# Kernel optimization log

Measured on AMD Instinct MI355X. Metric: run time of the kernel, lower is better.

The kernel has to match this reference:

```python
import jax, jax.numpy as jnp
import numpy as np

T, B, D, H = 1024, 64, 256, 256


def setup_inputs() -> dict:
    key = jax.random.key(0)
    ks = jax.random.split(key, 7)
    u = lambda k, shape: jax.random.uniform(k, shape, jnp.float32, -0.1, 0.1)
    x = jax.random.normal(ks[0], (T, B, D), dtype=jnp.float32)
    # gate order along last axis: f, g, i, o (each block of width H)
    fwd_W = u(ks[1], (D, 4 * H))
    fwd_U = u(ks[2], (H, 4 * H))
    fwd_b = u(ks[3], (4 * H,))
    bwd_W = u(ks[4], (D, 4 * H))
    bwd_U = u(ks[5], (H, 4 * H))
    bwd_b = u(ks[6], (4 * H,))
    return {"x": x, "fwd_W": fwd_W, "fwd_U": fwd_U, "fwd_b": fwd_b,
            "bwd_W": bwd_W, "bwd_U": bwd_U, "bwd_b": bwd_b}


def _lstm_scan(x, W, U, b):
    # x: [T, B, D]; returns (hs [T,B,H], h_last [B,H])
    Bsz = x.shape[1]
    h0 = jnp.zeros((Bsz, H), x.dtype)
    c0 = jnp.zeros((Bsz, H), x.dtype)
    xW = x @ W  # precompute input projections: [T, B, 4H]

    def step(carry, xw_t):
        h, c = carry
        z = xw_t + h @ U + b  # [B, 4H]
        f = jax.nn.sigmoid(z[:, 0 * H:1 * H])
        g = jnp.tanh(z[:, 1 * H:2 * H])
        i = jax.nn.sigmoid(z[:, 2 * H:3 * H])
        o = jax.nn.sigmoid(z[:, 3 * H:4 * H])
        c_new = c * f + g * i
        h_new = o * jnp.tanh(c_new)
        return (h_new, c_new), h_new

    (h_last, _), hs = jax.lax.scan(step, (h0, c0), xW)
    return hs, h_last


def reference(x, fwd_W, fwd_U, fwd_b, bwd_W, bwd_U, bwd_b):
    hs_f, h_f = _lstm_scan(x, fwd_W, fwd_U, fwd_b)
    hs_b_rev, h_b = _lstm_scan(x[::-1], bwd_W, bwd_U, bwd_b)
    hs_b = hs_b_rev[::-1]
    output = jnp.concatenate([hs_f, hs_b], axis=-1)  # [T, B, 2H]
    return (output, h_f, h_b)
```

## Files before the change

### kernel.cpp

```cpp
#include <hip/hip_runtime.h>

#define T_STEPS 1024
#define BATCH   64
#define NDIM    256
#define HID     256
#define G4      1024

typedef short bf16x8 __attribute__((ext_vector_type(8)));
typedef float f32x4  __attribute__((ext_vector_type(4)));
typedef unsigned short u16;

#define XW_ELEMS ((size_t)2 * T_STEPS * BATCH * G4)
#define UT_ELEMS ((size_t)2 * 4 * 65536)

__device__ __forceinline__ float b2f(u16 v) {
  union { unsigned u; float f; } c; c.u = ((unsigned)v) << 16; return c.f;
}
__device__ __forceinline__ u16 f2b(float f) {
  union { float f; unsigned u; } c; c.f = f;
  unsigned u = c.u;
  u += 0x7fffu + ((u >> 16) & 1u);
  return (u16)(u >> 16);
}
__device__ __forceinline__ float sigm(float x) {
  float e = __expf(-x);
  return __builtin_amdgcn_rcpf(1.0f + e);
}
__device__ __forceinline__ float tanh_f(float x) {
  return 2.0f * sigm(2.0f * x) - 1.0f;
}

__global__ __launch_bounds__(1024) void build_ut(
    const float* __restrict__ U0, const float* __restrict__ U1,
    u16* __restrict__ UT)
{
  const int d = blockIdx.x >> 2;
  const int g = blockIdx.x & 3;
  const float* __restrict__ U = d ? U1 : U0;
  const int w = threadIdx.x >> 6, lane = threadIdx.x & 63;
  const int q = lane >> 4, c15 = lane & 15;
  u16* dst = UT + ((size_t)d * 4 + g) * 65536;
  #pragma unroll
  for (int kf = 0; kf < 8; ++kf) {
    bf16x8 v;
    #pragma unroll
    for (int j = 0; j < 8; ++j)
      v[j] = (short)f2b(U[(size_t)(kf * 32 + q * 8 + j) * G4 + g * 256 + w * 16 + c15]);
    ((bf16x8*)dst)[((w * 8 + kf) << 6) + lane] = v;
  }
}

__global__ __launch_bounds__(256, 2) void xw_gemm(
    const float* __restrict__ x,
    const float* __restrict__ W0, const float* __restrict__ W1,
    const float* __restrict__ b0, const float* __restrict__ b1,
    u16* __restrict__ xw)
{
  const int d  = blockIdx.y >> 4;
  const int n0 = (blockIdx.y & 15) * 64;
  const int t0 = blockIdx.x * 32;
  const float* __restrict__ W    = d ? W1 : W0;
  const float* __restrict__ bias = d ? b1 : b0;
  const int lane = threadIdx.x & 63;
  const int wv   = threadIdx.x >> 6;
  const int q    = lane >> 4;
  const int c15  = lane & 15;

  bf16x8 uf[4][8];
  #pragma unroll
  for (int ct = 0; ct < 4; ++ct) {
    const int col = n0 + ct * 16 + c15;
    #pragma unroll
    for (int kf = 0; kf < 8; ++kf) {
      #pragma unroll
      for (int j = 0; j < 8; ++j)
        uf[ct][kf][j] = (short)f2b(W[(size_t)(kf * 32 + q * 8 + j) * G4 + col]);
    }
  }
  float bc[4];
  #pragma unroll
  for (int ct = 0; ct < 4; ++ct) bc[ct] = bias[n0 + ct * 16 + c15];

  __shared__ __align__(16) u16 Alds[64 * 256];

  for (int t = t0; t < t0 + 32; ++t) {
    __syncthreads();
    const float* xt = x + (size_t)t * BATCH * NDIM;
    #pragma unroll
    for (int i = 0; i < 8; ++i) {
      int g = (int)threadIdx.x + 256 * i;
      int r = g >> 5, c = g & 31;
      const float* src = xt + r * 256 + c * 8;
      bf16x8 v;
      #pragma unroll
      for (int j = 0; j < 8; ++j) v[j] = (short)f2b(src[j]);
      int cs = (c & 16) | ((c ^ (r & 15)) & 15);
      ((bf16x8*)Alds)[r * 32 + cs] = v;
    }
    __syncthreads();

    bf16x8 af[8];
    const int arow = wv * 16 + c15;
    #pragma unroll
    for (int kf = 0; kf < 8; ++kf) {
      int c = kf * 4 + q;
      int cs = (c & 16) | ((c ^ c15) & 15);
      af[kf] = ((const bf16x8*)Alds)[arow * 32 + cs];
    }

    f32x4 acc[4];
    #pragma unroll
    for (int ct = 0; ct < 4; ++ct) acc[ct] = (f32x4){0.f, 0.f, 0.f, 0.f};
    #pragma unroll
    for (int kf = 0; kf < 8; ++kf) {
      #pragma unroll
      for (int ct = 0; ct < 4; ++ct)
        acc[ct] = __builtin_amdgcn_mfma_f32_16x16x32_bf16(af[kf], uf[ct][kf], acc[ct], 0, 0, 0);
    }

    u16* dst = xw + (((size_t)d * T_STEPS + t) * 4 + wv) * 16384;
    #pragma unroll
    for (int ct = 0; ct < 4; ++ct) {
      int ncol = n0 + ct * 16;
      int g2 = ncol >> 8, w2 = (ncol >> 4) & 15;
      union { u16 s[4]; uint2 v; } pk;
      #pragma unroll
      for (int r = 0; r < 4; ++r) pk.s[r] = f2b(acc[ct][r] + bc[ct]);
      *(uint2*)(dst + (size_t)(w2 * 64 + q * 16 + c15) * 16 + g2 * 4) = pk.v;
    }
  }
}

__global__ __launch_bounds__(1024) void lstm_scan_fast(
    const u16* __restrict__ xw, const u16* __restrict__ UT,
    float* __restrict__ out)
{
  extern __shared__ __align__(16) u16 dynlds[];
  const int d  = blockIdx.x >> 2;
  const int bt = blockIdx.x & 3;
  const int tid  = threadIdx.x;
  const int w    = tid >> 6;
  const int lane = tid & 63;
  const int q    = lane >> 4;
  const int c15  = lane & 15;

  const u16* __restrict__ UTd = UT + (size_t)d * 4 * 65536;

  bf16x8 uf0[8], uf1[8];
  const bf16x8* UTf = (const bf16x8*)UTd;
  #pragma unroll
  for (int kf = 0; kf < 8; ++kf) {
    uf0[kf] = UTf[       ((w * 8 + kf) << 6) + lane];
    uf1[kf] = UTf[8192 + ((w * 8 + kf) << 6) + lane];
  }

  {
    const int4* src = (const int4*)(UTd + 2 * 65536);
    int4* dstl = (int4*)(dynlds + 8192);
    for (int i = tid; i < 8192; i += 1024) dstl[i] = src[i];
    for (int i = tid; i < 8192; i += 1024) dynlds[i] = 0;
  }

  const int4* __restrict__ Uo4 = (const int4*)(UTd + 3 * 65536);
  const int obase = (w << 9) | lane;
  const char* uib_base = (const char*)(dynlds + 8192) + (size_t)obase * 16;

  int afo[8];
  #pragma unroll
  for (int kf = 0; kf < 8; ++kf) {
    int cc = kf * 4 + q;
    int cs = (cc & 16) | ((cc ^ c15) & 15);
    afo[kf] = (c15 * 32 + cs) * 16;
  }
  const int colv = w * 16 + c15;
  int hwo[4];
  #pragma unroll
  for (int r = 0; r < 4; ++r) {
    int row = q * 4 + r;
    int cch = colv >> 3;
    int cs = (cch & 16) | ((cch ^ row) & 15);
    hwo[r] = ((row * 32 + cs) * 8 + (colv & 7)) * 2;
  }

  float cst[4] = {0.f, 0.f, 0.f, 0.f};
  __syncthreads();

  const int rowbase = bt * 16;
  const size_t hlast_base = (size_t)T_STEPS * BATCH * (2 * HID) + (size_t)d * BATCH * HID;
  const int t_first = d ? (T_STEPS - 1) : 0;

  const long xw_stride = d ? -(long)(4 * 16384) : (long)(4 * 16384);
  const u16* xwp = xw + (((size_t)d * T_STEPS + t_first) * 4 + bt) * 16384 + (size_t)tid * 16;
  union I4x2 { int4 v[2]; u16 s[16]; };
  I4x2 xn;
  xn.v[0] = ((const int4*)xwp)[0];
  xn.v[1] = ((const int4*)xwp)[1];
  xwp += xw_stride;

  int4 ofr[3];
  ofr[0] = Uo4[obase];
  ofr[1] = Uo4[obase + 64];

  float* outp = out + (size_t)(t_first * BATCH + rowbase + q * 4) * (2 * HID)
              + (size_t)d * HID + colv;
  const long out_stride = d ? -(long)(BATCH * 2 * HID) : (long)(BATCH * 2 * HID);

  int curoff = 0;
  for (int it = 0; it < T_STEPS; ++it) {
    f32x4 acc0 = { b2f(xn.s[0]),  b2f(xn.s[1]),  b2f(xn.s[2]),  b2f(xn.s[3])  };
    f32x4 acc1 = { b2f(xn.s[4]),  b2f(xn.s[5]),  b2f(xn.s[6]),  b2f(xn.s[7])  };
    f32x4 acc2 = { b2f(xn.s[8]),  b2f(xn.s[9]),  b2f(xn.s[10]), b2f(xn.s[11]) };
    f32x4 acc3 = { b2f(xn.s[12]), b2f(xn.s[13]), b2f(xn.s[14]), b2f(xn.s[15]) };

    if (it + 1 < T_STEPS) {
      xn.v[0] = ((const int4*)xwp)[0];
      xn.v[1] = ((const int4*)xwp)[1];
      xwp += xw_stride;
    }

    const char* hcb = (const char*)dynlds + curoff;
    bf16x8 afb[2], uib[2];
    afb[0] = *(const bf16x8*)(hcb + afo[0]);
    uib[0] = *(const bf16x8*)(uib_base);
    #pragma unroll
    for (int kf = 0; kf < 8; ++kf) {
      if (kf < 7) {
        afb[(kf + 1) & 1] = *(const bf16x8*)(hcb + afo[kf + 1]);
        uib[(kf + 1) & 1] = *(const bf16x8*)(uib_base + (kf + 1) * 1024);
      }
      if (kf < 6) ofr[(kf + 2) % 3] = Uo4[obase + ((kf + 2) << 6)];
      bf16x8 af = afb[kf & 1];
      union { int4 v; bf16x8 b; } oc; oc.v = ofr[kf % 3];
      acc0 = __builtin_amdgcn_mfma_f32_16x16x32_bf16(af, uf0[kf],     acc0, 0, 0, 0);
      acc1 = __builtin_amdgcn_mfma_f32_16x16x32_bf16(af, uf1[kf],     acc1, 0, 0, 0);
      acc2 = __builtin_amdgcn_mfma_f32_16x16x32_bf16(af, uib[kf & 1], acc2, 0, 0, 0);
      acc3 = __builtin_amdgcn_mfma_f32_16x16x32_bf16(af, oc.b,        acc3, 0, 0, 0);
    }
    ofr[0] = Uo4[obase];
    ofr[1] = Uo4[obase + 64];

    u16 hb[4]; float hv[4];
    #pragma unroll
    for (int r = 0; r < 4; ++r) {
      float fg = sigm(acc0[r]);
      float gg = tanh_f(acc1[r]);
      float ig = sigm(acc2[r]);
      float og = sigm(acc3[r]);
      float cn = cst[r] * fg + gg * ig;
      cst[r] = cn;
      hv[r] = og * tanh_f(cn);
      hb[r] = f2b(hv[r]);
    }

    const int nxtoff = curoff ^ 8192;
    char* hwp = (char*)dynlds + nxtoff;
    #pragma unroll
    for (int r = 0; r < 4; ++r) {
      *(u16*)(hwp + hwo[r]) = hb[r];
      outp[r * (2 * HID)] = hv[r];
    }
    outp += out_stride;
    if (it == T_STEPS - 1) {
      #pragma unroll
      for (int r = 0; r < 4; ++r)
        out[hlast_base + (size_t)(rowbase + q * 4 + r) * HID + colv] = hv[r];
    }
    curoff = nxtoff;
    __syncthreads();
  }
}

__global__ __launch_bounds__(1024) void lstm_scan_safe(
    const u16* __restrict__ xw,
    const float* __restrict__ U0, const float* __restrict__ U1,
    float* __restrict__ out)
{
  const int d  = blockIdx.x >> 2;
  const int bt = blockIdx.x & 3;
  const int tid  = threadIdx.x;
  const int w    = tid >> 6;
  const int lane = tid & 63;
  const int q    = lane >> 4;
  const int c15  = lane & 15;
  const float* __restrict__ U = d ? U1 : U0;

  bf16x8 uf[4][8];
  #pragma unroll
  for (int g = 0; g < 4; ++g) {
    const int col2 = g * 256 + w * 16 + c15;
    #pragma unroll
    for (int kf = 0; kf < 8; ++kf) {
      #pragma unroll
      for (int j = 0; j < 8; ++j)
        uf[g][kf][j] = (short)f2b(U[(size_t)(kf * 32 + q * 8 + j) * G4 + col2]);
    }
  }

  __shared__ __align__(16) u16 hbuf[2][16 * 256];
  for (int i = tid; i < 16 * 256; i += 1024) { hbuf[0][i] = 0; hbuf[1][i] = 0; }
  float cst[4] = {0.f, 0.f, 0.f, 0.f};
  __syncthreads();

  const int rowbase = bt * 16;
  const int col = w * 16 + c15;
  const size_t hlast_base = (size_t)T_STEPS * BATCH * (2 * HID) + (size_t)d * BATCH * HID;

  for (int it = 0; it < T_STEPS; ++it) {
    const int t = d ? (T_STEPS - 1 - it) : it;
    union { int4 v[2]; u16 s[16]; } xv;
    {
      const int4* xwt = (const int4*)(xw + ((((size_t)d * T_STEPS + t) * 4 + bt) * 1024 + tid) * 16);
      xv.v[0] = xwt[0]; xv.v[1] = xwt[1];
    }
    const int cur = it & 1;
    bf16x8 af[8];
    #pragma unroll
    for (int kf = 0; kf < 8; ++kf) {
      int cc = kf * 4 + q;
      int cs = (cc & 16) | ((cc ^ c15) & 15);
      af[kf] = ((const bf16x8*)hbuf[cur])[c15 * 32 + cs];
    }
    f32x4 acc[4];
    #pragma unroll
    for (int g = 0; g < 4; ++g) acc[g] = (f32x4){0.f, 0.f, 0.f, 0.f};
    #pragma unroll
    for (int kf = 0; kf < 8; ++kf)
      #pragma unroll
      for (int g = 0; g < 4; ++g)
        acc[g] = __builtin_amdgcn_mfma_f32_16x16x32_bf16(af[kf], uf[g][kf], acc[g], 0, 0, 0);

    u16 hb[4]; float hv[4];
    #pragma unroll
    for (int r = 0; r < 4; ++r) {
      float zf = acc[0][r] + b2f(xv.s[0 * 4 + r]);
      float zg = acc[1][r] + b2f(xv.s[1 * 4 + r]);
      float zi = acc[2][r] + b2f(xv.s[2 * 4 + r]);
      float zo = acc[3][r] + b2f(xv.s[3 * 4 + r]);
      float fg = sigm(zf), gg = tanh_f(zg), ig = sigm(zi), og = sigm(zo);
      float cn = cst[r] * fg + gg * ig;
      cst[r] = cn;
      hv[r] = og * tanh_f(cn);
      hb[r] = f2b(hv[r]);
    }
    const int nxt = cur ^ 1;
    #pragma unroll
    for (int r = 0; r < 4; ++r) {
      const int row = q * 4 + r;
      int cch = col >> 3;
      int cs = (cch & 16) | ((cch ^ row) & 15);
      hbuf[nxt][(row * 32 + cs) * 8 + (col & 7)] = hb[r];
      out[((size_t)t * BATCH + rowbase + row) * (2 * HID) + (size_t)d * HID + col] = hv[r];
    }
    if (it == T_STEPS - 1) {
      #pragma unroll
      for (int r = 0; r < 4; ++r)
        out[hlast_base + (size_t)(rowbase + q * 4 + r) * HID + col] = hv[r];
    }
    __syncthreads();
  }
}

extern "C" void kernel_launch(void* const* d_in, const int* in_sizes, int n_in,
                              void* d_out, int out_size, void* d_ws, size_t ws_size,
                              hipStream_t stream) {
  const float* x  = (const float*)d_in[0];
  const float* fW = (const float*)d_in[1];
  const float* fU = (const float*)d_in[2];
  const float* fb = (const float*)d_in[3];
  const float* bW = (const float*)d_in[4];
  const float* bU = (const float*)d_in[5];
  const float* bb = (const float*)d_in[6];
  u16*   xwbuf = (u16*)d_ws;
  u16*   UT    = (u16*)d_ws + XW_ELEMS;
  float* out   = (float*)d_out;

  const bool fast = ws_size >= (XW_ELEMS + UT_ELEMS) * sizeof(u16);

  dim3 g1(32, 32);
  xw_gemm<<<g1, 256, 0, stream>>>(x, fW, bW, fb, bb, xwbuf);
  if (fast) {
    build_ut<<<8, 1024, 0, stream>>>(fU, bU, UT);
    hipFuncSetAttribute((const void*)lstm_scan_fast,
                        hipFuncAttributeMaxDynamicSharedMemorySize, 147456);
    lstm_scan_fast<<<8, 1024, 147456, stream>>>(xwbuf, UT, out);
  } else {
    lstm_scan_safe<<<8, 1024, 0, stream>>>(xwbuf, fU, bU, out);
  }
}
```

Baseline: 3.915 ms.

## Fold log2e scaling into weights and fuse LSTM gate math with fewer reciprocals

Pre-scales W, U and bias by log2(e), or 2·log2(e) for the tanh gate, so the recurrent loop can call exp2 directly without a multiply. The gate nonlinearities and cell update are combined algebraically, cutting five reciprocals per element to two. The h values are packed to bf16 with a hardware pack instruction, and the U_o/U_i fragment prefetch is restructured to a deeper rotation that is issued before the loop barrier. The changes shorten the serial per-step critical path of the recurrence, at the cost of overflow clamping concerns and a change in rounding behaviour.

```diff
diff --git a/kernel.cpp b/kernel.cpp
--- a/kernel.cpp
+++ b/kernel.cpp
@@ -6,6 +6,9 @@
 #define HID     256
 #define G4      1024
 
+#define L2E  1.4426950408889634f
+#define L2E2 2.8853900817779268f
+
 typedef short bf16x8 __attribute__((ext_vector_type(8)));
 typedef float f32x4  __attribute__((ext_vector_type(4)));
 typedef unsigned short u16;
@@ -21,13 +24,6 @@
   unsigned u = c.u;
   u += 0x7fffu + ((u >> 16) & 1u);
   return (u16)(u >> 16);
-}
-__device__ __forceinline__ float sigm(float x) {
-  float e = __expf(-x);
-  return __builtin_amdgcn_rcpf(1.0f + e);
-}
-__device__ __forceinline__ float tanh_f(float x) {
-  return 2.0f * sigm(2.0f * x) - 1.0f;
 }
 
 __global__ __launch_bounds__(1024) void build_ut(
@@ -36,6 +32,7 @@
 {
   const int d = blockIdx.x >> 2;
   const int g = blockIdx.x & 3;
+  const float sc = (g == 1) ? L2E2 : L2E;
   const float* __restrict__ U = d ? U1 : U0;
   const int w = threadIdx.x >> 6, lane = threadIdx.x & 63;
   const int q = lane >> 4, c15 = lane & 15;
@@ -45,7 +42,7 @@
     bf16x8 v;
     #pragma unroll
     for (int j = 0; j < 8; ++j)
-      v[j] = (short)f2b(U[(size_t)(kf * 32 + q * 8 + j) * G4 + g * 256 + w * 16 + c15]);
+      v[j] = (short)f2b(sc * U[(size_t)(kf * 32 + q * 8 + j) * G4 + g * 256 + w * 16 + c15]);
     ((bf16x8*)dst)[((w * 8 + kf) << 6) + lane] = v;
   }
 }
@@ -67,19 +64,19 @@
   const int c15  = lane & 15;
 
   bf16x8 uf[4][8];
+  float bc[4];
   #pragma unroll
   for (int ct = 0; ct < 4; ++ct) {
     const int col = n0 + ct * 16 + c15;
+    const float sc = (((n0 + ct * 16) >> 8) == 1) ? L2E2 : L2E;
     #pragma unroll
     for (int kf = 0; kf < 8; ++kf) {
       #pragma unroll
       for (int j = 0; j < 8; ++j)
-        uf[ct][kf][j] = (short)f2b(W[(size_t)(kf * 32 + q * 8 + j) * G4 + col]);
-    }
-  }
-  float bc[4];
-  #pragma unroll
-  for (int ct = 0; ct < 4; ++ct) bc[ct] = bias[n0 + ct * 16 + c15];
+        uf[ct][kf][j] = (short)f2b(sc * W[(size_t)(kf * 32 + q * 8 + j) * G4 + col]);
+    }
+    bc[ct] = sc * bias[col];
+  }
 
   __shared__ __align__(16) u16 Alds[64 * 256];
 
@@ -200,6 +197,10 @@
   int4 ofr[3];
   ofr[0] = Uo4[obase];
   ofr[1] = Uo4[obase + 64];
+  ofr[2] = Uo4[obase + 128];
+
+  bf16x8 uib[2];
+  uib[0] = *(const bf16x8*)(uib_base);
 
   float* outp = out + (size_t)(t_first * BATCH + rowbase + q * 4) * (2 * HID)
               + (size_t)d * HID + colv;
@@ -219,18 +220,17 @@
     }
 
     const char* hcb = (const char*)dynlds + curoff;
-    bf16x8 afb[2], uib[2];
+    bf16x8 afb[2];
     afb[0] = *(const bf16x8*)(hcb + afo[0]);
-    uib[0] = *(const bf16x8*)(uib_base);
     #pragma unroll
     for (int kf = 0; kf < 8; ++kf) {
       if (kf < 7) {
         afb[(kf + 1) & 1] = *(const bf16x8*)(hcb + afo[kf + 1]);
         uib[(kf + 1) & 1] = *(const bf16x8*)(uib_base + (kf + 1) * 1024);
       }
-      if (kf < 6) ofr[(kf + 2) % 3] = Uo4[obase + ((kf + 2) << 6)];
+      union { int4 v; bf16x8 b; } oc; oc.v = ofr[kf % 3];
+      if (kf < 5) ofr[kf % 3] = Uo4[obase + ((kf + 3) << 6)];
       bf16x8 af = afb[kf & 1];
-      union { int4 v; bf16x8 b; } oc; oc.v = ofr[kf % 3];
       acc0 = __builtin_amdgcn_mfma_f32_16x16x32_bf16(af, uf0[kf],     acc0, 0, 0, 0);
       acc1 = __builtin_amdgcn_mfma_f32_16x16x32_bf16(af, uf1[kf],     acc1, 0, 0, 0);
       acc2 = __builtin_amdgcn_mfma_f32_16x16x32_bf16(af, uib[kf & 1], acc2, 0, 0, 0);
@@ -238,19 +238,28 @@
     }
     ofr[0] = Uo4[obase];
     ofr[1] = Uo4[obase + 64];
-
-    u16 hb[4]; float hv[4];
+    ofr[2] = Uo4[obase + 128];
+
+    float hv[4];
     #pragma unroll
     for (int r = 0; r < 4; ++r) {
-      float fg = sigm(acc0[r]);
-      float gg = tanh_f(acc1[r]);
-      float ig = sigm(acc2[r]);
-      float og = sigm(acc3[r]);
-      float cn = cst[r] * fg + gg * ig;
+      float ef = __builtin_amdgcn_exp2f(-acc0[r]);
+      float eg = __builtin_amdgcn_exp2f(-acc1[r]);
+      float ei = __builtin_amdgcn_exp2f(-acc2[r]);
+      float eo = __builtin_amdgcn_exp2f(-acc3[r]);
+      float A = 1.0f + ef, B = 1.0f + eg, C = 1.0f + ei, D = 1.0f - eg;
+      float BC  = B * C;
+      float num = cst[r] * BC + D * A;
+      float cn  = num * __builtin_amdgcn_rcpf(A * BC);
       cst[r] = cn;
-      hv[r] = og * tanh_f(cn);
-      hb[r] = f2b(hv[r]);
-    }
+      float ec = __builtin_amdgcn_exp2f(fminf(-L2E2 * cn, 30.0f));
+      float E = 1.0f + eo, F = 1.0f + ec, G = 1.0f - ec;
+      hv[r] = G * __builtin_amdgcn_rcpf(E * F);
+    }
+    unsigned p01, p23;
+    asm("v_cvt_pk_bf16_f32 %0, %1, %2" : "=v"(p01) : "v"(hv[0]), "v"(hv[1]));
+    asm("v_cvt_pk_bf16_f32 %0, %1, %2" : "=v"(p23) : "v"(hv[2]), "v"(hv[3]));
+    u16 hb[4] = { (u16)p01, (u16)(p01 >> 16), (u16)p23, (u16)(p23 >> 16) };
 
     const int nxtoff = curoff ^ 8192;
     char* hwp = (char*)dynlds + nxtoff;
@@ -266,6 +275,7 @@
         out[hlast_base + (size_t)(rowbase + q * 4 + r) * HID + colv] = hv[r];
     }
     curoff = nxtoff;
+    uib[0] = *(const bf16x8*)(uib_base);
     __syncthreads();
   }
 }
@@ -288,11 +298,12 @@
   #pragma unroll
   for (int g = 0; g < 4; ++g) {
     const int col2 = g * 256 + w * 16 + c15;
+    const float sc = (g == 1) ? L2E2 : L2E;
     #pragma unroll
     for (int kf = 0; kf < 8; ++kf) {
       #pragma unroll
       for (int j = 0; j < 8; ++j)
-        uf[g][kf][j] = (short)f2b(U[(size_t)(kf * 32 + q * 8 + j) * G4 + col2]);
+        uf[g][kf][j] = (short)f2b(sc * U[(size_t)(kf * 32 + q * 8 + j) * G4 + col2]);
     }
   }
 
@@ -336,10 +347,18 @@
       float zg = acc[1][r] + b2f(xv.s[1 * 4 + r]);
       float zi = acc[2][r] + b2f(xv.s[2 * 4 + r]);
       float zo = acc[3][r] + b2f(xv.s[3 * 4 + r]);
-      float fg = sigm(zf), gg = tanh_f(zg), ig = sigm(zi), og = sigm(zo);
-      float cn = cst[r] * fg + gg * ig;
+      float ef = __builtin_amdgcn_exp2f(-zf);
+      float eg = __builtin_amdgcn_exp2f(-zg);
+      float ei = __builtin_amdgcn_exp2f(-zi);
+      float eo = __builtin_amdgcn_exp2f(-zo);
+      float A = 1.0f + ef, B = 1.0f + eg, C = 1.0f + ei, D = 1.0f - eg;
+      float BC  = B * C;
+      float num = cst[r] * BC + D * A;
+      float cn  = num * __builtin_amdgcn_rcpf(A * BC);
       cst[r] = cn;
-      hv[r] = og * tanh_f(cn);
+      float ec = __builtin_amdgcn_exp2f(fminf(-L2E2 * cn, 30.0f));
+      float E = 1.0f + eo, F = 1.0f + ec, G = 1.0f - ec;
+      hv[r] = G * __builtin_amdgcn_rcpf(E * F);
       hb[r] = f2b(hv[r]);
     }
     const int nxt = cur ^ 1;
```

Result: slower. 4.420 ms (+12.9%).

## Pre-pack input weights to bf16 and restructure input projection GEMM around time tiles

Applied to the files above, without the earlier changes.

Adds a pre-pass that converts both input weight matrices to bf16 in the MFMA fragment layout, reusing the recurrent-weight packing kernel. A new projection kernel has each block load two timesteps of x into swizzled LDS once, keep the A fragments in registers, and loop over all 32 output column tiles for both directions. Weight fragments are read straight from global memory. The aim is to avoid repeatedly converting fp32 weights and re-reading x across blocks, at the cost of an extra launch, extra workspace and heavier register use.

```diff
diff --git a/kernel.cpp b/kernel.cpp
--- a/kernel.cpp
+++ b/kernel.cpp
@@ -12,6 +12,7 @@
 
 #define XW_ELEMS ((size_t)2 * T_STEPS * BATCH * G4)
 #define UT_ELEMS ((size_t)2 * 4 * 65536)
+#define WT_ELEMS UT_ELEMS
 
 __device__ __forceinline__ float b2f(u16 v) {
   union { unsigned u; float f; } c; c.u = ((unsigned)v) << 16; return c.f;
@@ -47,6 +48,93 @@
     for (int j = 0; j < 8; ++j)
       v[j] = (short)f2b(U[(size_t)(kf * 32 + q * 8 + j) * G4 + g * 256 + w * 16 + c15]);
     ((bf16x8*)dst)[((w * 8 + kf) << 6) + lane] = v;
+  }
+}
+
+__global__ __launch_bounds__(256, 2) void xw_gemm_v2(
+    const float* __restrict__ x,
+    const u16* __restrict__ WT,
+    const float* __restrict__ b0, const float* __restrict__ b1,
+    u16* __restrict__ xw)
+{
+  const int t0   = blockIdx.x * 2;
+  const int lane = threadIdx.x & 63;
+  const int wv   = threadIdx.x >> 6;
+  const int q    = lane >> 4;
+  const int c15  = lane & 15;
+
+  __shared__ __align__(16) u16 Alds[2 * 64 * 256];
+
+  #pragma unroll
+  for (int t01 = 0; t01 < 2; ++t01) {
+    const float* xt = x + (size_t)(t0 + t01) * BATCH * NDIM;
+    #pragma unroll
+    for (int i = 0; i < 8; ++i) {
+      int g = (int)threadIdx.x + 256 * i;
+      int r = g >> 5, c = g & 31;
+      const float* src = xt + r * 256 + c * 8;
+      bf16x8 v;
+      #pragma unroll
+      for (int j = 0; j < 8; ++j) v[j] = (short)f2b(src[j]);
+      int cs = (c & 16) | ((c ^ (r & 15)) & 15);
+      ((bf16x8*)Alds)[t01 * 2048 + r * 32 + cs] = v;
+    }
+  }
+  __syncthreads();
+
+  bf16x8 af2[2][8];
+  const int arow = wv * 16 + c15;
+  #pragma unroll
+  for (int t01 = 0; t01 < 2; ++t01) {
+    #pragma unroll
+    for (int kf = 0; kf < 8; ++kf) {
+      int c = kf * 4 + q;
+      int cs = (c & 16) | ((c ^ c15) & 15);
+      af2[t01][kf] = ((const bf16x8*)Alds)[t01 * 2048 + arow * 32 + cs];
+    }
+  }
+
+  for (int iter = 0; iter < 32; ++iter) {
+    const int d  = iter >> 4;
+    const int n0 = (iter & 15) * 64;
+    const float* __restrict__ bias = d ? b1 : b0;
+
+    bf16x8 uf[4][8];
+    float bc[4];
+    #pragma unroll
+    for (int ct = 0; ct < 4; ++ct) {
+      const int ncol = n0 + ct * 16;
+      const int g2 = ncol >> 8, wcol = (ncol >> 4) & 15;
+      const bf16x8* wsrc = (const bf16x8*)(WT + ((size_t)d * 4 + g2) * 65536);
+      #pragma unroll
+      for (int kf = 0; kf < 8; ++kf)
+        uf[ct][kf] = wsrc[((wcol * 8 + kf) << 6) + lane];
+      bc[ct] = bias[ncol + c15];
+    }
+
+    #pragma unroll
+    for (int t01 = 0; t01 < 2; ++t01) {
+      f32x4 acc[4];
+      #pragma unroll
+      for (int ct = 0; ct < 4; ++ct) acc[ct] = (f32x4){0.f, 0.f, 0.f, 0.f};
+      #pragma unroll
+      for (int kf = 0; kf < 8; ++kf) {
+        #pragma unroll
+        for (int ct = 0; ct < 4; ++ct)
+          acc[ct] = __builtin_amdgcn_mfma_f32_16x16x32_bf16(af2[t01][kf], uf[ct][kf], acc[ct], 0, 0, 0);
+      }
+
+      u16* dst = xw + (((size_t)d * T_STEPS + (t0 + t01)) * 4 + wv) * 16384;
+      #pragma unroll
+      for (int ct = 0; ct < 4; ++ct) {
+        int ncol = n0 + ct * 16;
+        int g2 = ncol >> 8, w2 = (ncol >> 4) & 15;
+        union { u16 s[4]; uint2 v; } pk;
+        #pragma unroll
+        for (int r = 0; r < 4; ++r) pk.s[r] = f2b(acc[ct][r] + bc[ct]);
+        *(uint2*)(dst + (size_t)(w2 * 64 + q * 16 + c15) * 16 + g2 * 4) = pk.v;
+      }
+    }
   }
 }
 
@@ -372,12 +460,19 @@
   const float* bb = (const float*)d_in[6];
   u16*   xwbuf = (u16*)d_ws;
   u16*   UT    = (u16*)d_ws + XW_ELEMS;
+  u16*   WT    = (u16*)d_ws + XW_ELEMS + UT_ELEMS;
   float* out   = (float*)d_out;
 
-  const bool fast = ws_size >= (XW_ELEMS + UT_ELEMS) * sizeof(u16);
-
-  dim3 g1(32, 32);
-  xw_gemm<<<g1, 256, 0, stream>>>(x, fW, bW, fb, bb, xwbuf);
+  const bool fast   = ws_size >= (XW_ELEMS + UT_ELEMS) * sizeof(u16);
+  const bool use_v2 = ws_size >= (XW_ELEMS + UT_ELEMS + WT_ELEMS) * sizeof(u16);
+
+  if (use_v2) {
+    build_ut<<<8, 1024, 0, stream>>>(fW, bW, WT);
+    xw_gemm_v2<<<512, 256, 0, stream>>>(x, WT, fb, bb, xwbuf);
+  } else {
+    dim3 g1(32, 32);
+    xw_gemm<<<g1, 256, 0, stream>>>(x, fW, bW, fb, bb, xwbuf);
+  }
   if (fast) {
     build_ut<<<8, 1024, 0, stream>>>(fU, bU, UT);
     hipFuncSetAttribute((const void*)lstm_scan_fast,
```

New measurement: 3.977 ms. Within noise of the previous version (+1.6%).
